# Optimization experiments

Hardware: AMD Instinct MI355X
Metric: run time of the kernel (lower is better)

## Reference

```python
import jax, jax.numpy as jnp
import numpy as np

N = 100000   # nodes
E = 3200000  # edges (avg degree 32)
IN = 512
HID = 128
OUT = 128


def setup_inputs() -> dict:
    key = jax.random.key(0)
    ks = jax.random.split(key, 9)
    x = jax.random.normal(ks[0], (N, IN), dtype=jnp.float32)
    edge_index = jax.random.randint(ks[1], (2, E), 0, N, dtype=jnp.int32)
    perm = jax.random.permutation(ks[2], N).astype(jnp.int32)
    # GCN layer params (glorot-ish scaling)
    W1 = jax.random.normal(ks[3], (IN, HID), jnp.float32) / np.sqrt(IN)
    b1 = jnp.zeros((HID,), jnp.float32)
    W2 = jax.random.normal(ks[4], (HID, OUT), jnp.float32) / np.sqrt(HID)
    b2 = jnp.zeros((OUT,), jnp.float32)
    # nn.Bilinear(OUT, OUT, 1): weight [1, OUT, OUT], bias [1]
    Wd = jax.random.normal(ks[5], (1, OUT, OUT), jnp.float32) / np.sqrt(OUT)
    bd = jnp.zeros((1,), jnp.float32)
    return {"x": x, "edge_index": edge_index, "perm": perm,
            "W1": W1, "b1": b1, "W2": W2, "b2": b2, "Wd": Wd, "bd": bd}


def gcn_conv(x, W, b, src, dst, n):
    """PyG GCNConv: add self-loops, symmetric deg^-1/2 norm, linear, scatter-add, bias."""
    h = x @ W  # [N, out]
    loops = jnp.arange(n, dtype=src.dtype)
    s = jnp.concatenate([src, loops])
    d = jnp.concatenate([dst, loops])
    deg = jax.ops.segment_sum(jnp.ones(d.shape, x.dtype), d, num_segments=n)
    dinv = jnp.where(deg > 0, jax.lax.rsqrt(deg), 0.0)
    norm = dinv[s] * dinv[d]                      # [E+N]
    msg = h[s] * norm[:, None]                     # gather + scale
    out = jax.ops.segment_sum(msg, d, num_segments=n)  # scatter-add to dst
    return out + b


def encode(x, W1, b1, W2, b2, src, dst, n):
    h = jax.nn.relu(gcn_conv(x, W1, b1, src, dst, n))
    return gcn_conv(h, W2, b2, src, dst, n)


def reference(x, edge_index, perm, W1, b1, W2, b2, Wd, bd):
    n = x.shape[0]
    src, dst = edge_index[0], edge_index[1]
    H = encode(x, W1, b1, W2, b2, src, dst, n)          # [N, OUT]
    s = jax.nn.sigmoid(jnp.mean(H, axis=0))             # [OUT]
    # Bilinear disc against broadcasted summary: pos[n] = H[n] @ Wd[0] @ s + bd
    Ws = Wd[0] @ s                                      # [OUT]
    pos = (H @ Ws)[:, None] + bd                        # [N, 1]
    Hc = encode(x[perm], W1, b1, W2, b2, src, dst, n)
    neg = (Hc @ Ws)[:, None] + bd                       # [N, 1]
    return pos, neg
```

## Files before the change

kernel.cpp:

```cpp
#include <hip/hip_runtime.h>
#include <hip/hip_bf16.h>

typedef unsigned int uint;
typedef unsigned short ushort;
typedef __attribute__((ext_vector_type(8))) short bf16x8;
typedef __attribute__((ext_vector_type(4))) float f32x4;

static __device__ __forceinline__ ushort f2bf(float f) {
    uint u = __builtin_bit_cast(uint, f);
    return (ushort)((u + 0x7FFFu + ((u >> 16) & 1u)) >> 16);
}
static __device__ __forceinline__ uint pk2(float lo, float hi) {
    return (uint)f2bf(lo) | ((uint)f2bf(hi) << 16);
}
static __device__ __forceinline__ float bflo(uint u) { return __builtin_bit_cast(float, u << 16); }
static __device__ __forceinline__ float bfhi(uint u) { return __builtin_bit_cast(float, u & 0xFFFF0000u); }


#define CS_G 512

__global__ __launch_bounds__(256) void part_hist_dual(
        const int* __restrict__ src, const int* __restrict__ dst,
        uint* __restrict__ counts, int E, int NB, int chunk) {
    __shared__ uint h0[512], h1[512];
    int t = threadIdx.x;
    for (int b = t; b < 512; b += 256) { h0[b] = 0; h1[b] = 0; }
    __syncthreads();
    int s0 = blockIdx.x * chunk;
    int s1 = min(s0 + chunk, E);
    int i = s0 + t * 4;
    for (; i + 4 <= s1; i += 1024) {
        int4 d4 = *(const int4*)(dst + i);
        int4 s4 = *(const int4*)(src + i);
        atomicAdd(&h0[d4.x >> 8], 1u); atomicAdd(&h0[d4.y >> 8], 1u);
        atomicAdd(&h0[d4.z >> 8], 1u); atomicAdd(&h0[d4.w >> 8], 1u);
        atomicAdd(&h1[s4.x >> 8], 1u); atomicAdd(&h1[s4.y >> 8], 1u);
        atomicAdd(&h1[s4.z >> 8], 1u); atomicAdd(&h1[s4.w >> 8], 1u);
    }
    for (int k = i; k < min(i + 4, s1); ++k) {
        atomicAdd(&h0[dst[k] >> 8], 1u);
        atomicAdd(&h1[src[k] >> 8], 1u);
    }
    __syncthreads();
    for (int b = t; b < NB; b += 256) {
        counts[(size_t)b * CS_G + blockIdx.x] = h0[b];
        counts[(size_t)(NB + b) * CS_G + blockIdx.x] = h1[b];
    }
}

__global__ __launch_bounds__(256) void part_scatter_dual(
        const int* __restrict__ src, const int* __restrict__ dst,
        const uint* __restrict__ scn, uint* __restrict__ rec,
        int E, int NB, int chunk) {
    __shared__ uint cur0[512], cur1[512];
    int t = threadIdx.x;
    for (int b = t; b < NB; b += 256) {
        cur0[b] = scn[(size_t)b * CS_G + blockIdx.x];
        cur1[b] = scn[(size_t)(NB + b) * CS_G + blockIdx.x];
    }
    __syncthreads();
    int s0 = blockIdx.x * chunk;
    int s1 = min(s0 + chunk, E);
    int i = s0 + t * 4;
    for (; i + 4 <= s1; i += 1024) {
        int4 d4 = *(const int4*)(dst + i);
        int4 s4 = *(const int4*)(src + i);
        int dd[4] = {d4.x, d4.y, d4.z, d4.w};
        int ss[4] = {s4.x, s4.y, s4.z, s4.w};
#pragma unroll
        for (int k = 0; k < 4; ++k) {
            uint slotD = atomicAdd(&cur0[dd[k] >> 8], 1u);
            rec[slotD] = ((uint)(dd[k] & 255) << 24) | (uint)ss[k];
            uint slotS = atomicAdd(&cur1[ss[k] >> 8], 1u);
            rec[slotS] = ((uint)(ss[k] & 255) << 24) | (uint)dd[k];
        }
    }
    for (int k = i; k < min(i + 4, s1); ++k) {
        int d = dst[k], s = src[k];
        uint slotD = atomicAdd(&cur0[d >> 8], 1u);
        rec[slotD] = ((uint)(d & 255) << 24) | (uint)s;
        uint slotS = atomicAdd(&cur1[s >> 8], 1u);
        rec[slotS] = ((uint)(s & 255) << 24) | (uint)d;
    }
}

__global__ __launch_bounds__(256) void bucket_build(
        const uint* __restrict__ scn, const uint* __restrict__ rec,
        int* __restrict__ rp, int* __restrict__ adj,
        float* __restrict__ dinv, int NB, int n) {
    __shared__ uint cnt[256];
    __shared__ uint sc[2][256];
    int b = blockIdx.x, t = threadIdx.x;
    uint base = scn[(size_t)b * CS_G];
    uint bend = scn[(size_t)(b + 1) * CS_G];
    cnt[t] = 0;
    __syncthreads();
    for (uint i = base + t; i < bend; i += 256)
        atomicAdd(&cnt[rec[i] >> 24], 1u);
    __syncthreads();
    uint vcnt = cnt[t];
    float dv = rsqrtf((float)(vcnt + 1));
    sc[0][t] = vcnt;
    __syncthreads();
    int pb = 0;
    for (int off = 1; off < 256; off <<= 1) {
        uint add = (t >= off) ? sc[pb][t - off] : 0u;
        sc[pb ^ 1][t] = sc[pb][t] + add;
        pb ^= 1;
        __syncthreads();
    }
    uint excl = sc[pb][t] - vcnt;
    uint off0 = base + excl;
    int vtx = b * 256 + t;
    if (vtx < n) {
        rp[vtx] = (int)off0;
        dinv[vtx] = dv;
    }
    if (b == 0 && t == 0) rp[n] = (int)scn[(size_t)NB * CS_G];
    cnt[t] = off0;
    __syncthreads();
    for (uint i = base + t; i < bend; i += 256) {
        uint r = rec[i];
        uint slot = atomicAdd(&cnt[r >> 24], 1u);
        adj[slot] = (int)(r & 0xFFFFFFu);
    }
}

__global__ __launch_bounds__(256) void bucket_tw_colsum(
        const uint* __restrict__ scn, const uint* __restrict__ rec,
        const float* __restrict__ dinv, const ushort* __restrict__ B,
        float* __restrict__ mBvec, int NB, int n) {
    __shared__ float tw_sh[256];
    __shared__ float tv_sh[256];
    __shared__ float sh[4][128];
    int b = blockIdx.x, t = threadIdx.x;
    uint base = scn[(size_t)(NB + b) * CS_G];
    uint bend = scn[(size_t)(NB + b + 1) * CS_G];
    tw_sh[t] = 0.f;
    __syncthreads();
    for (uint i = base + t; i < bend; i += 256) {
        uint r = rec[i];
        atomicAdd(&tw_sh[r >> 24], dinv[r & 0xFFFFFFu]);
    }
    __syncthreads();
    int vtx = b * 256 + t;
    float dv = (vtx < n) ? dinv[vtx] : 0.f;
    tv_sh[t] = dv * (tw_sh[t] + dv);
    __syncthreads();
    int cp = t & 63, rg = t >> 6;
    int rmax = min(256, n - b * 256);
    float acc0 = 0.f, acc1 = 0.f;
    for (int r = rg; r < rmax; r += 4) {
        float tv = tv_sh[r];
        uint bb = *(const uint*)(B + ((size_t)(b * 256 + r)) * 128 + 2 * cp);
        acc0 += bflo(bb) * tv;
        acc1 += bfhi(bb) * tv;
    }
    sh[rg][2 * cp] = acc0;
    sh[rg][2 * cp + 1] = acc1;
    __syncthreads();
    if (t < 128)
        atomicAdd(&mBvec[t], sh[0][t] + sh[1][t] + sh[2][t] + sh[3][t]);
}


#define SC_T 256
#define SC_C 1024

__global__ void scan_part(const int* __restrict__ deg, int* __restrict__ bsum, int n) {
    __shared__ int sh[SC_T];
    int t = threadIdx.x;
    int base = blockIdx.x * SC_C;
    int s = 0;
    for (int i = 0; i < 4; i++) {
        int idx = base + t * 4 + i;
        if (idx < n) s += deg[idx];
    }
    sh[t] = s;
    __syncthreads();
    for (int off = 128; off > 0; off >>= 1) {
        if (t < off) sh[t] += sh[t + off];
        __syncthreads();
    }
    if (t == 0) bsum[blockIdx.x] = sh[0];
}

__global__ void scan_block(int* bsum, int nb, int* total) {
    __shared__ int sh[256];
    int t = threadIdx.x;
    int v[4];
    int s = 0;
#pragma unroll
    for (int i = 0; i < 4; i++) {
        int idx = t * 4 + i;
        v[i] = (idx < nb) ? bsum[idx] : 0;
        s += v[i];
    }
    sh[t] = s;
    __syncthreads();
    for (int off = 1; off < 256; off <<= 1) {
        int u = (t >= off) ? sh[t - off] : 0;
        __syncthreads();
        sh[t] += u;
        __syncthreads();
    }
    int excl = sh[t] - s;
#pragma unroll
    for (int i = 0; i < 4; i++) {
        int idx = t * 4 + i;
        if (idx < nb) { bsum[idx] = excl; excl += v[i]; }
    }
    if (t == 255) *total = sh[255];
}

__global__ void scan_write(const int* __restrict__ deg, const int* __restrict__ bsum,
                           const int* __restrict__ total, int* __restrict__ rp, int n) {
    __shared__ int sh[SC_T];
    int t = threadIdx.x;
    int base = blockIdx.x * SC_C;
    int vals[4];
    int s = 0;
    for (int i = 0; i < 4; i++) {
        int idx = base + t * 4 + i;
        vals[i] = (idx < n) ? deg[idx] : 0;
        s += vals[i];
    }
    sh[t] = s;
    __syncthreads();
    for (int off = 1; off < SC_T; off <<= 1) {
        int v = (t >= off) ? sh[t - off] : 0;
        __syncthreads();
        sh[t] += v;
        __syncthreads();
    }
    int excl = sh[t] - s + bsum[blockIdx.x];
    for (int i = 0; i < 4; i++) {
        int idx = base + t * 4 + i;
        if (idx < n) { rp[idx] = excl; excl += vals[i]; }
    }
    if (blockIdx.x == 0 && t == 0) rp[n] = *total;
}


__global__ void pack_w(const float* __restrict__ W, ushort* __restrict__ Wp) {
    int kc = blockIdx.x >> 3, n = blockIdx.x & 7;
    int l = threadIdx.x;
    ushort o[8];
#pragma unroll
    for (int j = 0; j < 8; ++j) {
        float v = W[(size_t)(kc * 32 + ((l >> 4) * 8) + j) * 128 + n * 16 + (l & 15)];
        o[j] = f2bf(v);
    }
    uint4 pk;
    pk.x = (uint)o[0] | ((uint)o[1] << 16);
    pk.y = (uint)o[2] | ((uint)o[3] << 16);
    pk.z = (uint)o[4] | ((uint)o[5] << 16);
    pk.w = (uint)o[6] | ((uint)o[7] << 16);
    *(uint4*)(Wp + ((size_t)(kc * 8 + n) * 64 + l) * 8) = pk;
}


__global__ __launch_bounds__(256) void gemm1_mfma(
        const float* __restrict__ X, const ushort* __restrict__ Wp,
        ushort* __restrict__ Cb, int M, int K) {
    __shared__ ushort As[2][64][40];
    int t = threadIdx.x, lane = t & 63, w = t >> 6;
    int brow = blockIdx.x * 64;
    int KC = K >> 5;
    f32x4 acc[8] = {};
    int sr = t >> 2, sk = (t & 3) * 8;
    int gr = brow + sr;
    bool xok = gr < M;
    int frow = w * 16 + (lane & 15);
    int fk = (lane >> 4) * 8;

    auto loadpk = [&](int kc) -> uint4 {
        float4 xa = make_float4(0.f, 0.f, 0.f, 0.f), xb = xa;
        if (xok) {
            const float* xp = X + (size_t)gr * K + kc * 32 + sk;
            xa = *(const float4*)xp;
            xb = *(const float4*)(xp + 4);
        }
        uint4 pk;
        pk.x = pk2(xa.x, xa.y);
        pk.y = pk2(xa.z, xa.w);
        pk.z = pk2(xb.x, xb.y);
        pk.w = pk2(xb.z, xb.w);
        return pk;
    };

    uint4 cur = loadpk(0);
    int buf = 0;
    for (int kc = 0; kc < KC; ++kc) {
        *(uint4*)&As[buf][sr][sk] = cur;
        __syncthreads();
        if (kc + 1 < KC) cur = loadpk(kc + 1);
        bf16x8 af = *(const bf16x8*)&As[buf][frow][fk];
        const ushort* wbase = Wp + ((size_t)(kc * 8) * 64 + lane) * 8;
#pragma unroll
        for (int n = 0; n < 8; ++n) {
            bf16x8 bfr = *(const bf16x8*)(wbase + (size_t)n * 64 * 8);
            acc[n] = __builtin_amdgcn_mfma_f32_16x16x32_bf16(af, bfr, acc[n], 0, 0, 0);
        }
        buf ^= 1;
    }
    int colbase = lane & 15;
    int rowbase = brow + w * 16 + ((lane >> 4) << 2);
#pragma unroll
    for (int n = 0; n < 8; ++n) {
#pragma unroll
        for (int r = 0; r < 4; ++r) {
            int grr = rowbase + r;
            if (grr < M) Cb[(size_t)grr * 128 + n * 16 + colbase] = f2bf(acc[n][r]);
        }
    }
}


#define ACC8(acc, g, w)                                   \
    acc[0] += bflo(g.x) * w; acc[1] += bfhi(g.x) * w;     \
    acc[2] += bflo(g.y) * w; acc[3] += bfhi(g.y) * w;     \
    acc[4] += bflo(g.z) * w; acc[5] += bfhi(g.z) * w;     \
    acc[6] += bflo(g.w) * w; acc[7] += bfhi(g.w) * w;

__global__ __launch_bounds__(256) void prop_b0(
        const ushort* __restrict__ A,
        const int* __restrict__ rp, const int* __restrict__ adj,
        const float* __restrict__ dinv, const float* __restrict__ bias,
        ushort* __restrict__ B, int n) {
    int wave = (blockIdx.x * blockDim.x + threadIdx.x) >> 6;
    int lane = threadIdx.x & 63;
    int q = lane >> 4, l = lane & 15;
    int v = wave * 4 + q;
    bool vok = v < n;
    int vc = vok ? v : (n - 1);
    float dv = dinv[vc];

    uint4 r0 = *(const uint4*)(A + (size_t)vc * 128 + 8 * l);
    float a0[8];
    a0[0] = bflo(r0.x) * dv; a0[1] = bfhi(r0.x) * dv;
    a0[2] = bflo(r0.y) * dv; a0[3] = bfhi(r0.y) * dv;
    a0[4] = bflo(r0.z) * dv; a0[5] = bfhi(r0.z) * dv;
    a0[6] = bflo(r0.w) * dv; a0[7] = bfhi(r0.w) * dv;

    int i = rp[vc], end = rp[vc + 1];
    int un[4];
#pragma unroll
    for (int k = 0; k < 4; ++k) un[k] = (i + k < end) ? adj[i + k] : vc;

    while (__ballot(i < end)) {
        int uc[4];
#pragma unroll
        for (int k = 0; k < 4; ++k) uc[k] = un[k];
        uint4 g0[4];
#pragma unroll
        for (int k = 0; k < 4; ++k) g0[k] = *(const uint4*)(A + (size_t)uc[k] * 128 + 8 * l);
        float du[4];
#pragma unroll
        for (int k = 0; k < 4; ++k) du[k] = (i + k < end) ? dinv[uc[k]] : 0.f;
        i += 4;
#pragma unroll
        for (int k = 0; k < 4; ++k) un[k] = (i + k < end) ? adj[i + k] : vc;
#pragma unroll
        for (int k = 0; k < 4; ++k) {
            float w = du[k];
            ACC8(a0, g0[k], w)
        }
    }
    if (!vok) return;
    float4 bA = *(const float4*)(bias + 8 * l);
    float4 bB = *(const float4*)(bias + 8 * l + 4);
    float bb[8] = {bA.x, bA.y, bA.z, bA.w, bB.x, bB.y, bB.z, bB.w};
#pragma unroll
    for (int j = 0; j < 8; ++j)
        a0[j] = fmaxf(a0[j] * dv + bb[j], 0.f);
    uint4 o;
    o.x = pk2(a0[0], a0[1]); o.y = pk2(a0[2], a0[3]);
    o.z = pk2(a0[4], a0[5]); o.w = pk2(a0[6], a0[7]);
    *(uint4*)(B + (size_t)v * 128 + 8 * l) = o;
}


__global__ __launch_bounds__(256) void prop_b1(
        const ushort* __restrict__ A, const ushort* __restrict__ B,
        const int* __restrict__ rp, const int* __restrict__ adj,
        const float* __restrict__ dinv, const int* __restrict__ perm,
        const float* __restrict__ bias, const float* __restrict__ w2s,
        float2* __restrict__ cpair, int n) {
    int wave = (blockIdx.x * blockDim.x + threadIdx.x) >> 6;
    int lane = threadIdx.x & 63;
    int q = lane >> 4, l = lane & 15;
    int v = wave * 4 + q;
    bool vok = v < n;
    int vc = vok ? v : (n - 1);
    float dv = dinv[vc];
    int self = perm[vc];

    uint4 r1 = *(const uint4*)(A + (size_t)self * 128 + 8 * l);
    float a1[8];
    a1[0] = bflo(r1.x) * dv; a1[1] = bfhi(r1.x) * dv;
    a1[2] = bflo(r1.y) * dv; a1[3] = bfhi(r1.y) * dv;
    a1[4] = bflo(r1.z) * dv; a1[5] = bfhi(r1.z) * dv;
    a1[6] = bflo(r1.w) * dv; a1[7] = bfhi(r1.w) * dv;

    int i = rp[vc], end = rp[vc + 1];
    int un[4];
#pragma unroll
    for (int k = 0; k < 4; ++k) un[k] = (i + k < end) ? adj[i + k] : vc;

    while (__ballot(i < end)) {
        int uc[4];
#pragma unroll
        for (int k = 0; k < 4; ++k) uc[k] = un[k];
        int uu[4];
#pragma unroll
        for (int k = 0; k < 4; ++k) uu[k] = perm[uc[k]];
        uint4 g1[4];
#pragma unroll
        for (int k = 0; k < 4; ++k) g1[k] = *(const uint4*)(A + (size_t)uu[k] * 128 + 8 * l);
        float du[4];
#pragma unroll
        for (int k = 0; k < 4; ++k) du[k] = (i + k < end) ? dinv[uc[k]] : 0.f;
        i += 4;
#pragma unroll
        for (int k = 0; k < 4; ++k) un[k] = (i + k < end) ? adj[i + k] : vc;
#pragma unroll
        for (int k = 0; k < 4; ++k) {
            float w = du[k];
            ACC8(a1, g1[k], w)
        }
    }
    if (!vok) return;
    float4 bA = *(const float4*)(bias + 8 * l);
    float4 bB = *(const float4*)(bias + 8 * l + 4);
    float bb[8] = {bA.x, bA.y, bA.z, bA.w, bB.x, bB.y, bB.z, bB.w};
    float4 wA = *(const float4*)(w2s + 8 * l);
    float4 wB = *(const float4*)(w2s + 8 * l + 4);
    float ww[8] = {wA.x, wA.y, wA.z, wA.w, wB.x, wB.y, wB.z, wB.w};
    float c1 = 0.f;
#pragma unroll
    for (int j = 0; j < 8; ++j)
        c1 += fmaxf(a1[j] * dv + bb[j], 0.f) * ww[j];
    uint4 b0 = *(const uint4*)(B + (size_t)vc * 128 + 8 * l);
    float c0 = bflo(b0.x) * ww[0] + bfhi(b0.x) * ww[1]
             + bflo(b0.y) * ww[2] + bfhi(b0.y) * ww[3]
             + bflo(b0.z) * ww[4] + bfhi(b0.z) * ww[5]
             + bflo(b0.w) * ww[6] + bfhi(b0.w) * ww[7];
#pragma unroll
    for (int off = 1; off < 16; off <<= 1) {
        c0 += __shfl_xor(c0, off);
        c1 += __shfl_xor(c1, off);
    }
    if (l == 0) cpair[v] = make_float2(dv * c0, dv * c1);
}


__global__ void tiny_chain(const float* __restrict__ mBvec, const float* __restrict__ W2,
                           const float* __restrict__ b2, const float* __restrict__ Wd,
                           const float* __restrict__ bd,
                           float* __restrict__ w2s, float* __restrict__ k0, int n) {
    __shared__ float s_sh[128];
    __shared__ float ws_sh[128];
    __shared__ float red[128];
    int t = threadIdx.x;
    float acc = 0.f;
    for (int k = 0; k < 128; ++k) acc += mBvec[k] * W2[k * 128 + t];
    float m = acc / (float)n + b2[t];
    s_sh[t] = 1.f / (1.f + expf(-m));
    __syncthreads();
    acc = 0.f;
    for (int j = 0; j < 128; ++j) acc += Wd[t * 128 + j] * s_sh[j];
    ws_sh[t] = acc;
    __syncthreads();
    acc = 0.f;
    for (int j = 0; j < 128; ++j) acc += W2[t * 128 + j] * ws_sh[j];
    w2s[t] = acc;
    red[t] = b2[t] * ws_sh[t];
    __syncthreads();
    for (int off = 64; off > 0; off >>= 1) {
        if (t < off) red[t] += red[t + off];
        __syncthreads();
    }
    if (t == 0) *k0 = red[0] + bd[0];
}

__global__ __launch_bounds__(256) void sprop(
        const float2* __restrict__ cpair,
        const int* __restrict__ rp, const int* __restrict__ adj,
        const float* __restrict__ dinv, const float* __restrict__ k0,
        float* __restrict__ out, int n) {
    int wave = (blockIdx.x * blockDim.x + threadIdx.x) >> 6;
    int lane = threadIdx.x & 63;
    int q = lane >> 4, l = lane & 15;
    int v = wave * 4 + q;
    if (v >= n) return;
    float a0 = 0.f, a1 = 0.f;
    int beg = rp[v], end = rp[v + 1];
    for (int i = beg + l; i < end; i += 16) {
        float2 c = cpair[adj[i]];
        a0 += c.x;
        a1 += c.y;
    }
#pragma unroll
    for (int off = 1; off < 16; off <<= 1) {
        a0 += __shfl_xor(a0, off);
        a1 += __shfl_xor(a1, off);
    }
    if (l == 0) {
        float dv = dinv[v];
        float kk = *k0;
        float2 cs = cpair[v];
        out[v] = dv * (a0 + cs.x) + kk;
        out[n + v] = dv * (a1 + cs.y) + kk;
    }
}


extern "C" void kernel_launch(void* const* d_in, const int* in_sizes, int n_in,
                              void* d_out, int out_size, void* d_ws, size_t ws_size,
                              hipStream_t stream) {
    const float* x  = (const float*)d_in[0];
    const int*   ei = (const int*)d_in[1];
    const int* perm = (const int*)d_in[2];
    const float* W1 = (const float*)d_in[3];
    const float* b1 = (const float*)d_in[4];
    const float* W2 = (const float*)d_in[5];
    const float* b2 = (const float*)d_in[6];
    const float* Wd = (const float*)d_in[7];
    const float* bd = (const float*)d_in[8];

    const int N = in_sizes[2];
    const int E = in_sizes[1] / 2;
    const int IN = in_sizes[0] / N;
    const int* src = ei;
    const int* dst = ei + E;
    float* out = (float*)d_out;

    const int NB = (N + 255) >> 8;
    const int M2 = 2 * NB * CS_G;
    int chunk = (E + CS_G - 1) / CS_G;
    chunk = (chunk + 3) & ~3;

    char* p = (char*)d_ws;
    auto alloc = [&](size_t bytes) -> void* {
        void* r = (void*)p;
        p += (bytes + 511) & ~(size_t)511;
        return r;
    };
    float* mBvec  = (float*)alloc(512);
    uint*  counts = (uint*)alloc((size_t)M2 * 4);
    uint*  scn    = (uint*)alloc((size_t)(M2 + 1) * 4);
    uint*  rec    = (uint*)alloc((size_t)2 * E * 4);
    int*   rp     = (int*)alloc((size_t)(N + 1) * 4);
    int*   adj    = (int*)alloc((size_t)E * 4);
    float* dinv   = (float*)alloc((size_t)N * 4);
    int*   bsum   = (int*)alloc(4096);
    int*   total  = (int*)alloc(64);
    float* w2sv   = (float*)alloc(512);
    float* k0v    = (float*)alloc(64);
    float2* cpair = (float2*)alloc((size_t)N * 8);
    ushort* W1p   = (ushort*)alloc((size_t)512 * 128 * 2);
    ushort* A  = (ushort*)alloc((size_t)N * 128 * 2);
    ushort* B  = (ushort*)alloc((size_t)N * 128 * 2);

    hipMemsetAsync(mBvec, 0, 512, stream);

    part_hist_dual<<<CS_G, 256, 0, stream>>>(src, dst, counts, E, NB, chunk);
    int nb_sc = (M2 + SC_C - 1) / SC_C;
    scan_part<<<nb_sc, SC_T, 0, stream>>>((const int*)counts, bsum, M2);
    scan_block<<<1, 256, 0, stream>>>(bsum, nb_sc, total);
    scan_write<<<nb_sc, SC_T, 0, stream>>>((const int*)counts, bsum, total, (int*)scn, M2);
    part_scatter_dual<<<CS_G, 256, 0, stream>>>(src, dst, scn, rec, E, NB, chunk);
    bucket_build<<<NB, 256, 0, stream>>>(scn, rec, rp, adj, dinv, NB, N);

    pack_w<<<(IN / 32) * 8, 64, 0, stream>>>(W1, W1p);

    int gemm_blocks = (N + 63) / 64;
    int p4_blocks = ((N + 3) / 4 + 3) / 4;

    gemm1_mfma<<<gemm_blocks, 256, 0, stream>>>(x, W1p, A, N, IN);
    prop_b0<<<p4_blocks, 256, 0, stream>>>(A, rp, adj, dinv, b1, B, N);
    bucket_tw_colsum<<<NB, 256, 0, stream>>>(scn, rec, dinv, B, mBvec, NB, N);
    tiny_chain<<<1, 128, 0, stream>>>(mBvec, W2, b2, Wd, bd, w2sv, k0v, N);
    prop_b1<<<p4_blocks, 256, 0, stream>>>(A, B, rp, adj, dinv, perm, b1, w2sv, cpair, N);
    sprop<<<p4_blocks, 256, 0, stream>>>(cpair, rp, adj, dinv, k0v, out, N);
}
```

Measured before the change: 505.4 us.

## Fuse weighted column-sum into first propagation kernel, precompute tv before GEMM

```diff
diff --git a/kernel.cpp b/kernel.cpp
--- a/kernel.cpp
+++ b/kernel.cpp
@@ -126,13 +126,11 @@
     }
 }
 
-__global__ __launch_bounds__(256) void bucket_tw_colsum(
+__global__ __launch_bounds__(256) void bucket_tw(
         const uint* __restrict__ scn, const uint* __restrict__ rec,
-        const float* __restrict__ dinv, const ushort* __restrict__ B,
-        float* __restrict__ mBvec, int NB, int n) {
+        const float* __restrict__ dinv, float* __restrict__ tv,
+        int NB, int n) {
     __shared__ float tw_sh[256];
-    __shared__ float tv_sh[256];
-    __shared__ float sh[4][128];
     int b = blockIdx.x, t = threadIdx.x;
     uint base = scn[(size_t)(NB + b) * CS_G];
     uint bend = scn[(size_t)(NB + b + 1) * CS_G];
@@ -144,23 +142,10 @@
     }
     __syncthreads();
     int vtx = b * 256 + t;
-    float dv = (vtx < n) ? dinv[vtx] : 0.f;
-    tv_sh[t] = dv * (tw_sh[t] + dv);
-    __syncthreads();
-    int cp = t & 63, rg = t >> 6;
-    int rmax = min(256, n - b * 256);
-    float acc0 = 0.f, acc1 = 0.f;
-    for (int r = rg; r < rmax; r += 4) {
-        float tv = tv_sh[r];
-        uint bb = *(const uint*)(B + ((size_t)(b * 256 + r)) * 128 + 2 * cp);
-        acc0 += bflo(bb) * tv;
-        acc1 += bfhi(bb) * tv;
-    }
-    sh[rg][2 * cp] = acc0;
-    sh[rg][2 * cp + 1] = acc1;
-    __syncthreads();
-    if (t < 128)
-        atomicAdd(&mBvec[t], sh[0][t] + sh[1][t] + sh[2][t] + sh[3][t]);
+    if (vtx < n) {
+        float dv = dinv[vtx];
+        tv[vtx] = dv * (tw_sh[t] + dv);
+    }
 }
 
 
@@ -326,10 +311,15 @@
 __global__ __launch_bounds__(256) void prop_b0(
         const ushort* __restrict__ A,
         const int* __restrict__ rp, const int* __restrict__ adj,
-        const float* __restrict__ dinv, const float* __restrict__ bias,
-        ushort* __restrict__ B, int n) {
-    int wave = (blockIdx.x * blockDim.x + threadIdx.x) >> 6;
-    int lane = threadIdx.x & 63;
+        const float* __restrict__ dinv, const float* __restrict__ tv,
+        const float* __restrict__ bias,
+        ushort* __restrict__ B, float* __restrict__ mparts, int n) {
+    __shared__ float msum[128];
+    int t = threadIdx.x;
+    if (t < 128) msum[t] = 0.f;
+    __syncthreads();
+    int wave = (blockIdx.x * blockDim.x + t) >> 6;
+    int lane = t & 63;
     int q = lane >> 4, l = lane & 15;
     int v = wave * 4 + q;
     bool vok = v < n;
@@ -367,17 +357,25 @@
             ACC8(a0, g0[k], w)
         }
     }
-    if (!vok) return;
     float4 bA = *(const float4*)(bias + 8 * l);
     float4 bB = *(const float4*)(bias + 8 * l + 4);
     float bb[8] = {bA.x, bA.y, bA.z, bA.w, bB.x, bB.y, bB.z, bB.w};
 #pragma unroll
     for (int j = 0; j < 8; ++j)
         a0[j] = fmaxf(a0[j] * dv + bb[j], 0.f);
-    uint4 o;
-    o.x = pk2(a0[0], a0[1]); o.y = pk2(a0[2], a0[3]);
-    o.z = pk2(a0[4], a0[5]); o.w = pk2(a0[6], a0[7]);
-    *(uint4*)(B + (size_t)v * 128 + 8 * l) = o;
+    if (vok) {
+        uint4 o;
+        o.x = pk2(a0[0], a0[1]); o.y = pk2(a0[2], a0[3]);
+        o.z = pk2(a0[4], a0[5]); o.w = pk2(a0[6], a0[7]);
+        *(uint4*)(B + (size_t)v * 128 + 8 * l) = o;
+    }
+    float tvv = vok ? tv[vc] : 0.f;
+#pragma unroll
+    for (int j = 0; j < 8; ++j)
+        atomicAdd(&msum[8 * l + j], tvv * a0[j]);
+    __syncthreads();
+    if (t < 128)
+        atomicAdd(&mparts[(size_t)(blockIdx.x & 31) * 128 + t], msum[t]);
 }
 
 
@@ -455,16 +453,21 @@
 }
 
 
-__global__ void tiny_chain(const float* __restrict__ mBvec, const float* __restrict__ W2,
+__global__ void tiny_chain(const float* __restrict__ mparts, const float* __restrict__ W2,
                            const float* __restrict__ b2, const float* __restrict__ Wd,
                            const float* __restrict__ bd,
                            float* __restrict__ w2s, float* __restrict__ k0, int n) {
+    __shared__ float mB[128];
     __shared__ float s_sh[128];
     __shared__ float ws_sh[128];
     __shared__ float red[128];
     int t = threadIdx.x;
     float acc = 0.f;
-    for (int k = 0; k < 128; ++k) acc += mBvec[k] * W2[k * 128 + t];
+    for (int r = 0; r < 32; ++r) acc += mparts[(size_t)r * 128 + t];
+    mB[t] = acc;
+    __syncthreads();
+    acc = 0.f;
+    for (int k = 0; k < 128; ++k) acc += mB[k] * W2[k * 128 + t];
     float m = acc / (float)n + b2[t];
     s_sh[t] = 1.f / (1.f + expf(-m));
     __syncthreads();
@@ -547,13 +550,14 @@
         p += (bytes + 511) & ~(size_t)511;
         return r;
     };
-    float* mBvec  = (float*)alloc(512);
+    float* mparts = (float*)alloc(32 * 128 * 4);
     uint*  counts = (uint*)alloc((size_t)M2 * 4);
     uint*  scn    = (uint*)alloc((size_t)(M2 + 1) * 4);
     uint*  rec    = (uint*)alloc((size_t)2 * E * 4);
     int*   rp     = (int*)alloc((size_t)(N + 1) * 4);
     int*   adj    = (int*)alloc((size_t)E * 4);
     float* dinv   = (float*)alloc((size_t)N * 4);
+    float* tvv    = (float*)alloc((size_t)N * 4);
     int*   bsum   = (int*)alloc(4096);
     int*   total  = (int*)alloc(64);
     float* w2sv   = (float*)alloc(512);
@@ -563,7 +567,7 @@
     ushort* A  = (ushort*)alloc((size_t)N * 128 * 2);
     ushort* B  = (ushort*)alloc((size_t)N * 128 * 2);
 
-    hipMemsetAsync(mBvec, 0, 512, stream);
+    hipMemsetAsync(mparts, 0, 32 * 128 * 4, stream);
 
     part_hist_dual<<<CS_G, 256, 0, stream>>>(src, dst, counts, E, NB, chunk);
     int nb_sc = (M2 + SC_C - 1) / SC_C;
@@ -572,6 +576,7 @@
     scan_write<<<nb_sc, SC_T, 0, stream>>>((const int*)counts, bsum, total, (int*)scn, M2);
     part_scatter_dual<<<CS_G, 256, 0, stream>>>(src, dst, scn, rec, E, NB, chunk);
     bucket_build<<<NB, 256, 0, stream>>>(scn, rec, rp, adj, dinv, NB, N);
+    bucket_tw<<<NB, 256, 0, stream>>>(scn, rec, dinv, tvv, NB, N);
 
     pack_w<<<(IN / 32) * 8, 64, 0, stream>>>(W1, W1p);
 
@@ -579,9 +584,8 @@
     int p4_blocks = ((N + 3) / 4 + 3) / 4;
 
     gemm1_mfma<<<gemm_blocks, 256, 0, stream>>>(x, W1p, A, N, IN);
-    prop_b0<<<p4_blocks, 256, 0, stream>>>(A, rp, adj, dinv, b1, B, N);
-    bucket_tw_colsum<<<NB, 256, 0, stream>>>(scn, rec, dinv, B, mBvec, NB, N);
-    tiny_chain<<<1, 128, 0, stream>>>(mBvec, W2, b2, Wd, bd, w2sv, k0v, N);
+    prop_b0<<<p4_blocks, 256, 0, stream>>>(A, rp, adj, dinv, tvv, b1, B, mparts, N);
+    tiny_chain<<<1, 128, 0, stream>>>(mparts, W2, b2, Wd, bd, w2sv, k0v, N);
     prop_b1<<<p4_blocks, 256, 0, stream>>>(A, B, rp, adj, dinv, perm, b1, w2sv, cpair, N);
     sprop<<<p4_blocks, 256, 0, stream>>>(cpair, rp, adj, dinv, k0v, out, N);
 }
```

After: 494.4 us. -2.2%, faster.
